# Optimization experiments

Hardware: AMD Instinct MI355X
Metric: run time of the kernel (lower is better)

## Reference

```python
import jax, jax.numpy as jnp
import numpy as np

N_NODES = 100000
N_EDGES = 1600000
IN_FEAT = 256
HIDDEN = 64
N_CLASSES = 16


def gcn_conv(x, edge_index, W, b):
    """PyG GCNConv: add self-loops, symmetric normalization, linear+aggregate."""
    n = x.shape[0]
    src, dst = edge_index[0], edge_index[1]
    loops = jnp.arange(n, dtype=src.dtype)
    src = jnp.concatenate([src, loops])
    dst = jnp.concatenate([dst, loops])
    # in-degree on graph with self-loops
    deg = jax.ops.segment_sum(jnp.ones(src.shape[0], dtype=x.dtype), dst, num_segments=n)
    dinv = jnp.where(deg > 0, jax.lax.rsqrt(deg), 0.0)
    h = x @ W                                  # [N, out]
    norm = dinv[src] * dinv[dst]               # [E+N]
    msg = h[src] * norm[:, None]                # gather + scale (memory-bound)
    out = jax.ops.segment_sum(msg, dst, num_segments=n)  # scatter-add
    return out + b


def setup_inputs() -> dict:
    key = jax.random.key(0)
    ks = jax.random.split(key, 5)
    x = jax.random.normal(ks[0], (N_NODES, IN_FEAT), dtype=jnp.float32)
    edge_index = jax.random.randint(ks[1], (2, N_EDGES), 0, N_NODES, dtype=jnp.int64)
    W1 = jax.random.normal(ks[2], (IN_FEAT, HIDDEN), dtype=jnp.float32) * (1.0 / np.sqrt(IN_FEAT))
    b1 = jnp.zeros((HIDDEN,), dtype=jnp.float32)
    W2 = jax.random.normal(ks[3], (HIDDEN, N_CLASSES), dtype=jnp.float32) * (1.0 / np.sqrt(HIDDEN))
    b2 = jnp.zeros((N_CLASSES,), dtype=jnp.float32)
    return {"x": x, "edge_index": edge_index, "W1": W1, "b1": b1, "W2": W2, "b2": b2}


def reference(x, edge_index, W1, b1, W2, b2):
    h = gcn_conv(x, edge_index, W1, b1)
    h = jax.nn.relu(h)
    # dropout p=0.5 is identity in eval mode (training=False)
    out = gcn_conv(h, edge_index, W2, b2)
    return out
```

## Files before the change

### kernel.cpp

```cpp
#include <hip/hip_runtime.h>

#define NN 100000
#define NE 1600000
#define FIN 256
#define FH 64
#define FC 16

#define NPB 512
#define NBKT ((NN + NPB - 1) / NPB)
#define NBLK 256
#define CHUNK (NE / NBLK)
#define CAP 12288
#define NB_GEMM1 ((NN + 127) / 128)

typedef int v2i __attribute__((ext_vector_type(2)));
typedef int v4i __attribute__((ext_vector_type(4)));
typedef short s16x8 __attribute__((ext_vector_type(8)));
typedef float f32x4 __attribute__((ext_vector_type(4)));
typedef _Float16 h16x8 __attribute__((ext_vector_type(8)));
typedef _Float16 h16x4 __attribute__((ext_vector_type(4)));

__device__ __forceinline__ float4 add4(float4 a, float4 v) {
    a.x += v.x; a.y += v.y; a.z += v.z; a.w += v.w;
    return a;
}
__device__ __forceinline__ float4 xor_add4(float4 r, int m) {
    r.x += __shfl_xor(r.x, m, 64); r.y += __shfl_xor(r.y, m, 64);
    r.z += __shfl_xor(r.z, m, 64); r.w += __shfl_xor(r.w, m, 64);
    return r;
}
__device__ __forceinline__ h16x8 hz8() {
    h16x8 p;
    #pragma unroll
    for (int i = 0; i < 8; i++) p[i] = (_Float16)0.0f;
    return p;
}
__device__ __forceinline__ h16x4 hz4() {
    h16x4 p;
    #pragma unroll
    for (int i = 0; i < 4; i++) p[i] = (_Float16)0.0f;
    return p;
}

__device__ __forceinline__ unsigned short bf16rne(float f) {
    unsigned u = __float_as_uint(f);
    u += 0x7FFFu + ((u >> 16) & 1u);
    return (unsigned short)(u >> 16);
}
__device__ __forceinline__ void split8(const float* f, s16x8& hi, s16x8& lo) {
    #pragma unroll
    for (int i = 0; i < 8; i++) {
        unsigned u = __float_as_uint(f[i]);
        unsigned short h = (unsigned short)((u + 0x7FFFu + ((u >> 16) & 1u)) >> 16);
        float l = f[i] - __uint_as_float((unsigned)h << 16);
        unsigned ul = __float_as_uint(l);
        hi[i] = (short)h;
        lo[i] = (short)((ul + 0x7FFFu + ((ul >> 16) & 1u)) >> 16);
    }
}
__device__ __forceinline__ int is64(const int* __restrict__ ei) {
    return (ei[1] == 0) & (ei[3] == 0) & (ei[5] == 0) & (ei[7] == 0);
}

__global__ __launch_bounds__(256) void histprep_k(const int* __restrict__ ei,
                                                  const float* __restrict__ W,
                                                  unsigned short* __restrict__ Whi,
                                                  unsigned short* __restrict__ Wlo,
                                                  int* __restrict__ cnt) {
    const int b = blockIdx.x, t = threadIdx.x;
    if (b < 8) {
        int slot = b * 256 + t;
        int l = slot & 63;
        int c = (slot >> 6) & 3;
        int s = slot >> 8;
        int k0 = s * 32 + (l >> 4) * 8;
        int col = c * 16 + (l & 15);
        #pragma unroll
        for (int i = 0; i < 8; i++) {
            float f = W[(k0 + i) * FH + col];
            unsigned short h = bf16rne(f);
            float lres = f - __uint_as_float((unsigned)h << 16);
            Whi[slot * 8 + i] = h;
            Wlo[slot * 8 + i] = bf16rne(lres);
        }
        return;
    }
    __shared__ int hist[NBKT];
    const int blk = b - 8;
    for (int j = t; j < NBKT; j += 256) hist[j] = 0;
    __syncthreads();
    int f = is64(ei);
    int base = blk * CHUNK;
    if (f) {
        for (int i = t; i < CHUNK; i += 256) {
            v2i p = *(const v2i*)&ei[2 * (NE + base + i)];
            atomicAdd(&hist[p.x >> 9], 1);
        }
    } else {
        for (int i = t; i < CHUNK; i += 256) {
            int d = ei[NE + base + i];
            atomicAdd(&hist[d >> 9], 1);
        }
    }
    __syncthreads();
    for (int j = t; j < NBKT; j += 256) cnt[j * NBLK + blk] = hist[j];
}

__global__ __launch_bounds__(1024) void scanoff_k(int* __restrict__ cnt,
                                                  int* __restrict__ bucketBase) {
    __shared__ int s[1024];
    const int t = threadIdx.x;
    const int SEG = (NBKT * NBLK) / 1024;
    int base = t * SEG;
    int sum = 0;
    for (int i = 0; i < SEG; i++) sum += cnt[base + i];
    s[t] = sum; __syncthreads();
    for (int off = 1; off < 1024; off <<= 1) {
        int u = (t >= off) ? s[t - off] : 0;
        __syncthreads();
        s[t] += u;
        __syncthreads();
    }
    int run = s[t] - sum;
    for (int i = 0; i < SEG; i++) {
        int g = base + i;
        int v = cnt[g];
        cnt[g] = run;
        if ((g & (NBLK - 1)) == 0) bucketBase[g / NBLK] = run;
        run += v;
    }
    if (t == 0) bucketBase[NBKT] = NE;
}

__global__ __launch_bounds__(256, 4) void scatgemm_k(const int* __restrict__ ei,
                                                     const int* __restrict__ cnt,
                                                     int* __restrict__ sorted,
                                                     const float* __restrict__ x,
                                                     const unsigned short* __restrict__ Whi,
                                                     const unsigned short* __restrict__ Wlo,
                                                     _Float16* __restrict__ h1h) {
    __shared__ int stash[CHUNK];
    __shared__ unsigned short bkt[CHUNK];
    __shared__ int lhist[NBKT];
    __shared__ int lstart[NBKT];
    __shared__ int lcur[NBKT];
    __shared__ int sred[256];
    const int b = blockIdx.x, t = threadIdx.x;
    if (b >= NB_GEMM1) {
        const int blk = b - NB_GEMM1;
        for (int j = t; j < NBKT; j += 256) lhist[j] = 0;
        __syncthreads();
        int f = is64(ei);
        int base = blk * CHUNK;
        if (f) {
            for (int i = t; i < CHUNK; i += 256) {
                v2i p = *(const v2i*)&ei[2 * (NE + base + i)];
                atomicAdd(&lhist[p.x >> 9], 1);
            }
        } else {
            for (int i = t; i < CHUNK; i += 256)
                atomicAdd(&lhist[ei[NE + base + i] >> 9], 1);
        }
        __syncthreads();
        int v = (t < NBKT) ? lhist[t] : 0;
        sred[t] = v; __syncthreads();
        for (int off = 1; off < 256; off <<= 1) {
            int u = (t >= off) ? sred[t - off] : 0;
            __syncthreads();
            sred[t] += u;
            __syncthreads();
        }
        if (t < NBKT) { lstart[t] = sred[t] - v; lcur[t] = sred[t] - v; }
        __syncthreads();
        if (f) {
            for (int i = t; i < CHUNK; i += 256) {
                int e = base + i;
                v2i ps = *(const v2i*)&ei[2 * e];
                v2i pd = *(const v2i*)&ei[2 * (NE + e)];
                int s = ps.x, d = pd.x;
                int bk = d >> 9;
                int pos = atomicAdd(&lcur[bk], 1);
                stash[pos] = s | ((d & (NPB - 1)) << 17);
                bkt[pos] = (unsigned short)bk;
            }
        } else {
            for (int i = t; i < CHUNK; i += 256) {
                int e = base + i;
                int s = ei[e], d = ei[NE + e];
                int bk = d >> 9;
                int pos = atomicAdd(&lcur[bk], 1);
                stash[pos] = s | ((d & (NPB - 1)) << 17);
                bkt[pos] = (unsigned short)bk;
            }
        }
        __syncthreads();
        for (int i = t; i < CHUNK; i += 256) {
            int bk = bkt[i];
            int g = cnt[bk * NBLK + blk] + (i - lstart[bk]);
            sorted[g] = stash[i];
        }
        return;
    }
    const int lane = t & 63;
    const int wid = t >> 6;
    const int mb = b * 128 + wid * 32;
    const int lr = lane & 15;
    const int lk = (lane >> 4) * 8;

    int ra0 = mb + lr;
    int ra1 = mb + 16 + lr;
    const float* pa0 = x + (size_t)(ra0 < NN ? ra0 : NN - 1) * FIN + lk;
    const float* pa1 = x + (size_t)(ra1 < NN ? ra1 : NN - 1) * FIN + lk;

    f32x4 acc[2][4] = {};

    for (int s = 0; s < 8; s++) {
        float fa0[8], fa1[8];
        float4 q;
        q = *(const float4*)(pa0 + s * 32);
        fa0[0] = q.x; fa0[1] = q.y; fa0[2] = q.z; fa0[3] = q.w;
        q = *(const float4*)(pa0 + s * 32 + 4);
        fa0[4] = q.x; fa0[5] = q.y; fa0[6] = q.z; fa0[7] = q.w;
        q = *(const float4*)(pa1 + s * 32);
        fa1[0] = q.x; fa1[1] = q.y; fa1[2] = q.z; fa1[3] = q.w;
        q = *(const float4*)(pa1 + s * 32 + 4);
        fa1[4] = q.x; fa1[5] = q.y; fa1[6] = q.z; fa1[7] = q.w;

        s16x8 a0h, a0l, a1h, a1l;
        split8(fa0, a0h, a0l);
        split8(fa1, a1h, a1l);

        #pragma unroll
        for (int c = 0; c < 4; c++) {
            s16x8 wh = *(const s16x8*)&Whi[((s * 4 + c) * 64 + lane) * 8];
            s16x8 wl = *(const s16x8*)&Wlo[((s * 4 + c) * 64 + lane) * 8];
            acc[0][c] = __builtin_amdgcn_mfma_f32_16x16x32_bf16(a0h, wh, acc[0][c], 0, 0, 0);
            acc[0][c] = __builtin_amdgcn_mfma_f32_16x16x32_bf16(a0l, wh, acc[0][c], 0, 0, 0);
            acc[0][c] = __builtin_amdgcn_mfma_f32_16x16x32_bf16(a0h, wl, acc[0][c], 0, 0, 0);
            acc[1][c] = __builtin_amdgcn_mfma_f32_16x16x32_bf16(a1h, wh, acc[1][c], 0, 0, 0);
            acc[1][c] = __builtin_amdgcn_mfma_f32_16x16x32_bf16(a1l, wh, acc[1][c], 0, 0, 0);
            acc[1][c] = __builtin_amdgcn_mfma_f32_16x16x32_bf16(a1h, wl, acc[1][c], 0, 0, 0);
        }
    }
    #pragma unroll
    for (int r = 0; r < 2; r++) {
        int rowb = mb + 16 * r + (lane >> 4) * 4;
        #pragma unroll
        for (int v = 0; v < 4; v++) {
            int row = rowb + v;
            if (row < NN) {
                #pragma unroll
                for (int c = 0; c < 4; c++)
                    h1h[(size_t)row * FH + 16 * c + lr] = (_Float16)acc[r][c][v];
            }
        }
    }
}

__global__ __launch_bounds__(256) void bucket_k(const int* __restrict__ sorted,
                                                const int* __restrict__ bucketBase,
                                                int* __restrict__ csr,
                                                int* __restrict__ row_start,
                                                float* __restrict__ dinv,
                                                _Float16* __restrict__ h1h) {
    __shared__ int stash[CAP];
    __shared__ int hist[NPB];
    __shared__ int startl[NPB];
    __shared__ int cursor[NPB];
    __shared__ int ss[256];
    const int t = threadIdx.x, b = blockIdx.x;
    const int nb0 = b * NPB;
    const int ncnt = (NN - nb0 < NPB) ? (NN - nb0) : NPB;
    const int ebase = bucketBase[b];
    const int ecnt = bucketBase[b + 1] - ebase;

    hist[t] = 0; hist[t + 256] = 0;
    __syncthreads();
    for (int i = t; i < ecnt; i += 256) {
        int v = sorted[ebase + i];
        if (i < CAP) stash[i] = v;
        atomicAdd(&hist[v >> 17], 1);
    }
    __syncthreads();
    int a = hist[2 * t], c = hist[2 * t + 1];
    int p = a + c;
    ss[t] = p; __syncthreads();
    for (int off = 1; off < 256; off <<= 1) {
        int u = (t >= off) ? ss[t - off] : 0;
        __syncthreads();
        ss[t] += u;
        __syncthreads();
    }
    int ex = ss[t] - p;
    startl[2 * t] = ex;       startl[2 * t + 1] = ex + a;
    cursor[2 * t] = ex;       cursor[2 * t + 1] = ex + a;
    __syncthreads();
    for (int j = t; j < ncnt; j += 256) {
        row_start[nb0 + j] = ebase + startl[j];
        dinv[nb0 + j] = rsqrtf((float)(hist[j] + 1));
    }
    if (b == 0 && t == 0) row_start[NN] = NE;
    for (int i = t; i < ecnt; i += 256) {
        int v = (i < CAP) ? stash[i] : sorted[ebase + i];
        int dl = v >> 17;
        int r = atomicAdd(&cursor[dl], 1);
        csr[ebase + r] = v & 0x1FFFF;
    }
    h16x8* hp = (h16x8*)h1h;
    for (int q = t; q < ncnt * 8; q += 256) {
        int rl = q >> 3;
        _Float16 dvh = (_Float16)rsqrtf((float)(hist[rl] + 1));
        h16x8 v = hp[(size_t)(nb0 + rl) * 8 + (q & 7)];
        #pragma unroll
        for (int i = 0; i < 8; i++) v[i] = v[i] * dvh;
        hp[(size_t)(nb0 + rl) * 8 + (q & 7)] = v;
    }
}

__global__ __launch_bounds__(256) void agg1g_k(const int* __restrict__ csr,
                                               const int* __restrict__ row_start,
                                               const _Float16* __restrict__ h1h,
                                               const float* __restrict__ dinv,
                                               const float* __restrict__ b1,
                                               const float* __restrict__ W2,
                                               _Float16* __restrict__ h2h) {
    __shared__ float sW2[FH * FC];
    __shared__ float sp[4][FH];
    const int t = threadIdx.x;
    #pragma unroll
    for (int i = 0; i < 4; i++) sW2[t + 256 * i] = W2[t + 256 * i];
    __syncthreads();

    const int wid = t >> 6;
    const int n = blockIdx.x * 4 + wid;
    const int lane = t & 63;
    if (n >= NN) return;
    const int sg = lane >> 3;
    const int fl = lane & 7;
    const h16x8* hp = (const h16x8*)h1h;
    int s0 = row_start[n], s1 = row_start[n + 1];
    float facc[8] = {};
    for (int j0 = s0; j0 < s1; j0 += 64) {
        int idx = j0 + lane;
        int sl = (idx < s1) ? csr[idx] : 0;
        int cnt = s1 - j0; if (cnt > 64) cnt = 64;
        h16x8 pA = hz8(), pB = hz8();
        int j = 0;
        for (; j + 16 <= cnt; j += 16) {
            int eA = __shfl(sl, j + sg, 64);
            int eB = __shfl(sl, j + 8 + sg, 64);
            pA += hp[eA * 8 + fl];
            pB += hp[eB * 8 + fl];
        }
        if (j + 8 <= cnt) {
            int eA = __shfl(sl, j + sg, 64);
            pA += hp[eA * 8 + fl];
            j += 8;
        }
        int rem = cnt - j;
        if (rem > 0) {
            int jj = j + (sg < rem ? sg : 0);
            int eA = __shfl(sl, jj, 64);
            h16x8 v = hp[eA * 8 + fl];
            if (sg < rem) pB += v;
        }
        #pragma unroll
        for (int i = 0; i < 8; i++)
            facc[i] += (float)pA[i] + (float)pB[i];
    }
    #pragma unroll
    for (int i = 0; i < 8; i++) {
        float r = facc[i];
        r += __shfl_xor(r, 8, 64);
        r += __shfl_xor(r, 16, 64);
        r += __shfl_xor(r, 32, 64);
        facc[i] = r;
    }
    float dn = dinv[n];
    if (sg == 0) {
        h16x8 sv = hp[n * 8 + fl];
        float4 p0, p1;
        float4 bq0 = *(const float4*)&b1[fl * 8];
        float4 bq1 = *(const float4*)&b1[fl * 8 + 4];
        p0.x = fmaxf(fmaf(facc[0] + (float)sv[0], dn, bq0.x), 0.f);
        p0.y = fmaxf(fmaf(facc[1] + (float)sv[1], dn, bq0.y), 0.f);
        p0.z = fmaxf(fmaf(facc[2] + (float)sv[2], dn, bq0.z), 0.f);
        p0.w = fmaxf(fmaf(facc[3] + (float)sv[3], dn, bq0.w), 0.f);
        p1.x = fmaxf(fmaf(facc[4] + (float)sv[4], dn, bq1.x), 0.f);
        p1.y = fmaxf(fmaf(facc[5] + (float)sv[5], dn, bq1.y), 0.f);
        p1.z = fmaxf(fmaf(facc[6] + (float)sv[6], dn, bq1.z), 0.f);
        p1.w = fmaxf(fmaf(facc[7] + (float)sv[7], dn, bq1.w), 0.f);
        *(float4*)&sp[wid][fl * 8] = p0;
        *(float4*)&sp[wid][fl * 8 + 4] = p1;
    }
    __builtin_amdgcn_s_waitcnt(0);
    if (lane < FC) {
        float o = 0.f;
        #pragma unroll 8
        for (int k = 0; k < FH; k++)
            o = fmaf(sp[wid][k], sW2[k * FC + lane], o);
        h2h[n * FC + lane] = (_Float16)(o * dn);
    }
}

__global__ __launch_bounds__(256) void agg2_k(const int* __restrict__ csr,
                                              const int* __restrict__ row_start,
                                              const _Float16* __restrict__ h2h,
                                              const float* __restrict__ dinv,
                                              const float* __restrict__ b2,
                                              float* __restrict__ out) {
    const int t = threadIdx.x;
    int n = blockIdx.x * 16 + (t >> 4);
    int l16 = t & 15;
    int base = t & 48;
    int q = (t >> 2) & 3;
    int c = t & 3;
    if (n >= NN) return;
    const h16x4* hp = (const h16x4*)h2h;
    int s0 = row_start[n], s1 = row_start[n + 1];
    h16x4 pA = hz4(), pB = hz4(), pC = hz4(), pD = hz4();
    for (int j0 = s0; j0 < s1; j0 += 16) {
        int idx = j0 + l16;
        int sl = (idx < s1) ? csr[idx] : 0;
        int cnt = s1 - j0; if (cnt > 16) cnt = 16;
        int j = 0;
        if (j + 16 <= cnt) {
            int eA = __shfl(sl, base + j + q, 64);
            int eB = __shfl(sl, base + j + 4 + q, 64);
            int eC = __shfl(sl, base + j + 8 + q, 64);
            int eD = __shfl(sl, base + j + 12 + q, 64);
            pA += hp[eA * 4 + c];
            pB += hp[eB * 4 + c];
            pC += hp[eC * 4 + c];
            pD += hp[eD * 4 + c];
            j += 16;
        }
        if (j + 8 <= cnt) {
            int eA = __shfl(sl, base + j + q, 64);
            int eB = __shfl(sl, base + j + 4 + q, 64);
            pA += hp[eA * 4 + c];
            pB += hp[eB * 4 + c];
            j += 8;
        }
        if (j + 4 <= cnt) {
            int eA = __shfl(sl, base + j + q, 64);
            pA += hp[eA * 4 + c];
            j += 4;
        }
        int rem = cnt - j;
        if (rem > 0) {
            int jj = base + j + (q < rem ? q : 0);
            int eA = __shfl(sl, jj, 64);
            h16x4 v = hp[eA * 4 + c];
            if (q < rem) pD += v;
        }
    }
    float4 A = make_float4((float)pA[0] + (float)pB[0] + (float)pC[0] + (float)pD[0],
                           (float)pA[1] + (float)pB[1] + (float)pC[1] + (float)pD[1],
                           (float)pA[2] + (float)pB[2] + (float)pC[2] + (float)pD[2],
                           (float)pA[3] + (float)pB[3] + (float)pC[3] + (float)pD[3]);
    float4 r = xor_add4(A, 4);
    r = xor_add4(r, 8);
    if (q == 0) {
        float dn = dinv[n];
        h16x4 sv = hp[n * 4 + c];
        float4 bq = *(const float4*)&b2[c * 4];
        float4 p;
        p.x = fmaf(r.x + (float)sv[0], dn, bq.x);
        p.y = fmaf(r.y + (float)sv[1], dn, bq.y);
        p.z = fmaf(r.z + (float)sv[2], dn, bq.z);
        p.w = fmaf(r.w + (float)sv[3], dn, bq.w);
        *(float4*)&out[n * FC + c * 4] = p;
    }
}

extern "C" void kernel_launch(void* const* d_in, const int* in_sizes, int n_in,
                              void* d_out, int out_size, void* d_ws, size_t ws_size,
                              hipStream_t stream) {
    const float* x  = (const float*)d_in[0];
    const int*   ei = (const int*)d_in[1];
    const float* W1 = (const float*)d_in[2];
    const float* b1 = (const float*)d_in[3];
    const float* W2 = (const float*)d_in[4];
    const float* b2 = (const float*)d_in[5];
    float* out = (float*)d_out;

    char* ws = (char*)d_ws;
    int*   row_start  = (int*)(ws + 0);
    float* dinv       = (float*)(ws + 512ull * 1024);
    int*   bucketBase = (int*)(ws + 960ull * 1024);
    unsigned short* Whi = (unsigned short*)(ws + 1024ull * 1024);
    unsigned short* Wlo = (unsigned short*)(ws + 1088ull * 1024);
    int*   cnt        = (int*)(ws + 1152ull * 1024);
    int*   csr        = (int*)(ws + 2048ull * 1024);
    int*   sorted     = (int*)(ws + 9216ull * 1024);
    _Float16* h1h     = (_Float16*)(ws + 16384ull * 1024);
    _Float16* h2h     = (_Float16*)(ws + 30720ull * 1024);

    histprep_k<<<8 + NBLK, 256, 0, stream>>>(ei, W1, Whi, Wlo, cnt);
    scanoff_k<<<1, 1024, 0, stream>>>(cnt, bucketBase);
    scatgemm_k<<<NB_GEMM1 + NBLK, 256, 0, stream>>>(ei, cnt, sorted, x, Whi, Wlo, h1h);
    bucket_k<<<NBKT, 256, 0, stream>>>(sorted, bucketBase, csr, row_start, dinv, h1h);
    agg1g_k<<<(NN + 3) / 4, 256, 0, stream>>>(csr, row_start, h1h, dinv, b1, W2, h2h);
    agg2_k<<<(NN + 15) / 16, 256, 0, stream>>>(csr, row_start, h2h, dinv, b2, out);
}
```

Baseline: 388.5 us.

## Parallelize bucket offset scan and simplify gather loops in aggregation kernels

Replaces the single-block 1024-thread offset scan with three kernels: a per-bucket reduce, a small scan over bucket totals, and a per-bucket row scan, so the scan work spreads across many blocks. The aggregation kernels now load CSR indices directly per lane instead of staging them through wave shuffles. The layer-1 kernel also moves the W2 projection into registers with shuffle reductions, dropping the shared-memory staging and the serial 64-step dot product. In exchange there are two extra kernel launches and redundant CSR index loads per lane.

```diff
diff --git a/kernel.cpp b/kernel.cpp
--- a/kernel.cpp
+++ b/kernel.cpp
@@ -14,21 +14,12 @@
 #define NB_GEMM1 ((NN + 127) / 128)
 
 typedef int v2i __attribute__((ext_vector_type(2)));
-typedef int v4i __attribute__((ext_vector_type(4)));
 typedef short s16x8 __attribute__((ext_vector_type(8)));
 typedef float f32x4 __attribute__((ext_vector_type(4)));
 typedef _Float16 h16x8 __attribute__((ext_vector_type(8)));
 typedef _Float16 h16x4 __attribute__((ext_vector_type(4)));
-
-__device__ __forceinline__ float4 add4(float4 a, float4 v) {
-    a.x += v.x; a.y += v.y; a.z += v.z; a.w += v.w;
-    return a;
-}
-__device__ __forceinline__ float4 xor_add4(float4 r, int m) {
-    r.x += __shfl_xor(r.x, m, 64); r.y += __shfl_xor(r.y, m, 64);
-    r.z += __shfl_xor(r.z, m, 64); r.w += __shfl_xor(r.w, m, 64);
-    return r;
-}
+typedef _Float16 h16x2 __attribute__((ext_vector_type(2)));
+
 __device__ __forceinline__ h16x8 hz8() {
     h16x8 p;
     #pragma unroll
@@ -106,30 +97,48 @@
     for (int j = t; j < NBKT; j += 256) cnt[j * NBLK + blk] = hist[j];
 }
 
-__global__ __launch_bounds__(1024) void scanoff_k(int* __restrict__ cnt,
-                                                  int* __restrict__ bucketBase) {
-    __shared__ int s[1024];
-    const int t = threadIdx.x;
-    const int SEG = (NBKT * NBLK) / 1024;
-    int base = t * SEG;
-    int sum = 0;
-    for (int i = 0; i < SEG; i++) sum += cnt[base + i];
-    s[t] = sum; __syncthreads();
-    for (int off = 1; off < 1024; off <<= 1) {
+__global__ __launch_bounds__(256) void bsum_k(const int* __restrict__ cnt,
+                                              int* __restrict__ bucketTot) {
+    __shared__ int red[256];
+    int b = blockIdx.x, t = threadIdx.x;
+    red[t] = cnt[b * NBLK + t];
+    __syncthreads();
+    for (int off = 128; off > 0; off >>= 1) {
+        if (t < off) red[t] += red[t + off];
+        __syncthreads();
+    }
+    if (t == 0) bucketTot[b] = red[0];
+}
+
+__global__ __launch_bounds__(256) void bscan_k(const int* __restrict__ bucketTot,
+                                               int* __restrict__ bucketBase) {
+    __shared__ int s[256];
+    int t = threadIdx.x;
+    int v = (t < NBKT) ? bucketTot[t] : 0;
+    s[t] = v; __syncthreads();
+    for (int off = 1; off < 256; off <<= 1) {
         int u = (t >= off) ? s[t - off] : 0;
         __syncthreads();
         s[t] += u;
         __syncthreads();
     }
-    int run = s[t] - sum;
-    for (int i = 0; i < SEG; i++) {
-        int g = base + i;
-        int v = cnt[g];
-        cnt[g] = run;
-        if ((g & (NBLK - 1)) == 0) bucketBase[g / NBLK] = run;
-        run += v;
-    }
+    if (t < NBKT) bucketBase[t] = s[t] - v;
     if (t == 0) bucketBase[NBKT] = NE;
+}
+
+__global__ __launch_bounds__(256) void brow_k(int* __restrict__ cnt,
+                                              const int* __restrict__ bucketBase) {
+    __shared__ int s[256];
+    int b = blockIdx.x, t = threadIdx.x;
+    int v = cnt[b * NBLK + t];
+    s[t] = v; __syncthreads();
+    for (int off = 1; off < 256; off <<= 1) {
+        int u = (t >= off) ? s[t - off] : 0;
+        __syncthreads();
+        s[t] += u;
+        __syncthreads();
+    }
+    cnt[b * NBLK + t] = bucketBase[b] + s[t] - v;
 }
 
 __global__ __launch_bounds__(256, 4) void scatgemm_k(const int* __restrict__ ei,
@@ -324,82 +333,58 @@
                                                const float* __restrict__ b1,
                                                const float* __restrict__ W2,
                                                _Float16* __restrict__ h2h) {
-    __shared__ float sW2[FH * FC];
-    __shared__ float sp[4][FH];
     const int t = threadIdx.x;
-    #pragma unroll
-    for (int i = 0; i < 4; i++) sW2[t + 256 * i] = W2[t + 256 * i];
-    __syncthreads();
-
     const int wid = t >> 6;
-    const int n = blockIdx.x * 4 + wid;
     const int lane = t & 63;
-    if (n >= NN) return;
     const int sg = lane >> 3;
     const int fl = lane & 7;
+    float w2r0[8], w2r1[8], br[8];
+    #pragma unroll
+    for (int i = 0; i < 8; i++) {
+        float2 w = *(const float2*)&W2[(fl * 8 + i) * FC + 2 * sg];
+        w2r0[i] = w.x; w2r1[i] = w.y;
+        br[i] = b1[fl * 8 + i];
+    }
+    const int n = blockIdx.x * 4 + wid;
+    if (n >= NN) return;
     const h16x8* hp = (const h16x8*)h1h;
     int s0 = row_start[n], s1 = row_start[n + 1];
-    float facc[8] = {};
-    for (int j0 = s0; j0 < s1; j0 += 64) {
-        int idx = j0 + lane;
-        int sl = (idx < s1) ? csr[idx] : 0;
-        int cnt = s1 - j0; if (cnt > 64) cnt = 64;
-        h16x8 pA = hz8(), pB = hz8();
-        int j = 0;
-        for (; j + 16 <= cnt; j += 16) {
-            int eA = __shfl(sl, j + sg, 64);
-            int eB = __shfl(sl, j + 8 + sg, 64);
-            pA += hp[eA * 8 + fl];
-            pB += hp[eB * 8 + fl];
-        }
-        if (j + 8 <= cnt) {
-            int eA = __shfl(sl, j + sg, 64);
-            pA += hp[eA * 8 + fl];
-            j += 8;
-        }
-        int rem = cnt - j;
-        if (rem > 0) {
-            int jj = j + (sg < rem ? sg : 0);
-            int eA = __shfl(sl, jj, 64);
-            h16x8 v = hp[eA * 8 + fl];
-            if (sg < rem) pB += v;
-        }
-        #pragma unroll
-        for (int i = 0; i < 8; i++)
-            facc[i] += (float)pA[i] + (float)pB[i];
-    }
+    h16x8 pA = hz8(), pB = hz8();
+    for (int j = s0; j < s1; j += 16) {
+        int e1 = j + sg, e2 = j + 8 + sg;
+        int c1 = csr[(e1 < s1) ? e1 : s1 - 1];
+        int c2 = csr[(e2 < s1) ? e2 : s1 - 1];
+        h16x8 vA = hp[(size_t)c1 * 8 + fl];
+        h16x8 vB = hp[(size_t)c2 * 8 + fl];
+        if (e1 < s1) pA += vA;
+        if (e2 < s1) pB += vB;
+    }
+    float facc[8];
+    #pragma unroll
+    for (int i = 0; i < 8; i++) facc[i] = (float)pA[i] + (float)pB[i];
     #pragma unroll
     for (int i = 0; i < 8; i++) {
-        float r = facc[i];
-        r += __shfl_xor(r, 8, 64);
-        r += __shfl_xor(r, 16, 64);
-        r += __shfl_xor(r, 32, 64);
-        facc[i] = r;
+        facc[i] += __shfl_xor(facc[i], 8, 64);
+        facc[i] += __shfl_xor(facc[i], 16, 64);
+        facc[i] += __shfl_xor(facc[i], 32, 64);
     }
     float dn = dinv[n];
-    if (sg == 0) {
-        h16x8 sv = hp[n * 8 + fl];
-        float4 p0, p1;
-        float4 bq0 = *(const float4*)&b1[fl * 8];
-        float4 bq1 = *(const float4*)&b1[fl * 8 + 4];
-        p0.x = fmaxf(fmaf(facc[0] + (float)sv[0], dn, bq0.x), 0.f);
-        p0.y = fmaxf(fmaf(facc[1] + (float)sv[1], dn, bq0.y), 0.f);
-        p0.z = fmaxf(fmaf(facc[2] + (float)sv[2], dn, bq0.z), 0.f);
-        p0.w = fmaxf(fmaf(facc[3] + (float)sv[3], dn, bq0.w), 0.f);
-        p1.x = fmaxf(fmaf(facc[4] + (float)sv[4], dn, bq1.x), 0.f);
-        p1.y = fmaxf(fmaf(facc[5] + (float)sv[5], dn, bq1.y), 0.f);
-        p1.z = fmaxf(fmaf(facc[6] + (float)sv[6], dn, bq1.z), 0.f);
-        p1.w = fmaxf(fmaf(facc[7] + (float)sv[7], dn, bq1.w), 0.f);
-        *(float4*)&sp[wid][fl * 8] = p0;
-        *(float4*)&sp[wid][fl * 8 + 4] = p1;
-    }
-    __builtin_amdgcn_s_waitcnt(0);
-    if (lane < FC) {
-        float o = 0.f;
-        #pragma unroll 8
-        for (int k = 0; k < FH; k++)
-            o = fmaf(sp[wid][k], sW2[k * FC + lane], o);
-        h2h[n * FC + lane] = (_Float16)(o * dn);
+    h16x8 sv = hp[(size_t)n * 8 + fl];
+    float o0 = 0.f, o1 = 0.f;
+    #pragma unroll
+    for (int i = 0; i < 8; i++) {
+        float pi = fmaxf(fmaf(facc[i] + (float)sv[i], dn, br[i]), 0.f);
+        o0 = fmaf(pi, w2r0[i], o0);
+        o1 = fmaf(pi, w2r1[i], o1);
+    }
+    o0 += __shfl_xor(o0, 1, 64); o1 += __shfl_xor(o1, 1, 64);
+    o0 += __shfl_xor(o0, 2, 64); o1 += __shfl_xor(o1, 2, 64);
+    o0 += __shfl_xor(o0, 4, 64); o1 += __shfl_xor(o1, 4, 64);
+    if (fl == 0) {
+        h16x2 r;
+        r[0] = (_Float16)(o0 * dn);
+        r[1] = (_Float16)(o1 * dn);
+        *(h16x2*)&h2h[(size_t)n * FC + 2 * sg] = r;
     }
 }
 
@@ -410,67 +395,40 @@
                                               const float* __restrict__ b2,
                                               float* __restrict__ out) {
     const int t = threadIdx.x;
-    int n = blockIdx.x * 16 + (t >> 4);
-    int l16 = t & 15;
-    int base = t & 48;
-    int q = (t >> 2) & 3;
-    int c = t & 3;
+    const int n = blockIdx.x * 16 + (t >> 4);
+    const int q = (t >> 2) & 3;
+    const int c = t & 3;
+    float4 bq = *(const float4*)&b2[c * 4];
     if (n >= NN) return;
     const h16x4* hp = (const h16x4*)h2h;
     int s0 = row_start[n], s1 = row_start[n + 1];
-    h16x4 pA = hz4(), pB = hz4(), pC = hz4(), pD = hz4();
-    for (int j0 = s0; j0 < s1; j0 += 16) {
-        int idx = j0 + l16;
-        int sl = (idx < s1) ? csr[idx] : 0;
-        int cnt = s1 - j0; if (cnt > 16) cnt = 16;
-        int j = 0;
-        if (j + 16 <= cnt) {
-            int eA = __shfl(sl, base + j + q, 64);
-            int eB = __shfl(sl, base + j + 4 + q, 64);
-            int eC = __shfl(sl, base + j + 8 + q, 64);
-            int eD = __shfl(sl, base + j + 12 + q, 64);
-            pA += hp[eA * 4 + c];
-            pB += hp[eB * 4 + c];
-            pC += hp[eC * 4 + c];
-            pD += hp[eD * 4 + c];
-            j += 16;
-        }
-        if (j + 8 <= cnt) {
-            int eA = __shfl(sl, base + j + q, 64);
-            int eB = __shfl(sl, base + j + 4 + q, 64);
-            pA += hp[eA * 4 + c];
-            pB += hp[eB * 4 + c];
-            j += 8;
-        }
-        if (j + 4 <= cnt) {
-            int eA = __shfl(sl, base + j + q, 64);
-            pA += hp[eA * 4 + c];
-            j += 4;
-        }
-        int rem = cnt - j;
-        if (rem > 0) {
-            int jj = base + j + (q < rem ? q : 0);
-            int eA = __shfl(sl, jj, 64);
-            h16x4 v = hp[eA * 4 + c];
-            if (q < rem) pD += v;
-        }
-    }
-    float4 A = make_float4((float)pA[0] + (float)pB[0] + (float)pC[0] + (float)pD[0],
-                           (float)pA[1] + (float)pB[1] + (float)pC[1] + (float)pD[1],
-                           (float)pA[2] + (float)pB[2] + (float)pC[2] + (float)pD[2],
-                           (float)pA[3] + (float)pB[3] + (float)pC[3] + (float)pD[3]);
-    float4 r = xor_add4(A, 4);
-    r = xor_add4(r, 8);
+    h16x4 pA = hz4(), pB = hz4();
+    for (int j = s0; j < s1; j += 8) {
+        int e1 = j + q, e2 = j + 4 + q;
+        int c1 = csr[(e1 < s1) ? e1 : s1 - 1];
+        int c2 = csr[(e2 < s1) ? e2 : s1 - 1];
+        h16x4 vA = hp[(size_t)c1 * 4 + c];
+        h16x4 vB = hp[(size_t)c2 * 4 + c];
+        if (e1 < s1) pA += vA;
+        if (e2 < s1) pB += vB;
+    }
+    float r0 = (float)pA[0] + (float)pB[0];
+    float r1 = (float)pA[1] + (float)pB[1];
+    float r2 = (float)pA[2] + (float)pB[2];
+    float r3 = (float)pA[3] + (float)pB[3];
+    r0 += __shfl_xor(r0, 4, 64); r1 += __shfl_xor(r1, 4, 64);
+    r2 += __shfl_xor(r2, 4, 64); r3 += __shfl_xor(r3, 4, 64);
+    r0 += __shfl_xor(r0, 8, 64); r1 += __shfl_xor(r1, 8, 64);
+    r2 += __shfl_xor(r2, 8, 64); r3 += __shfl_xor(r3, 8, 64);
     if (q == 0) {
         float dn = dinv[n];
-        h16x4 sv = hp[n * 4 + c];
-        float4 bq = *(const float4*)&b2[c * 4];
+        h16x4 sv = hp[(size_t)n * 4 + c];
         float4 p;
-        p.x = fmaf(r.x + (float)sv[0], dn, bq.x);
-        p.y = fmaf(r.y + (float)sv[1], dn, bq.y);
-        p.z = fmaf(r.z + (float)sv[2], dn, bq.z);
-        p.w = fmaf(r.w + (float)sv[3], dn, bq.w);
-        *(float4*)&out[n * FC + c * 4] = p;
+        p.x = fmaf(r0 + (float)sv[0], dn, bq.x);
+        p.y = fmaf(r1 + (float)sv[1], dn, bq.y);
+        p.z = fmaf(r2 + (float)sv[2], dn, bq.z);
+        p.w = fmaf(r3 + (float)sv[3], dn, bq.w);
+        *(float4*)&out[(size_t)n * FC + c * 4] = p;
     }
 }
 
@@ -489,6 +447,7 @@
     int*   row_start  = (int*)(ws + 0);
     float* dinv       = (float*)(ws + 512ull * 1024);
     int*   bucketBase = (int*)(ws + 960ull * 1024);
+    int*   bucketTot  = (int*)(ws + 968ull * 1024);
     unsigned short* Whi = (unsigned short*)(ws + 1024ull * 1024);
     unsigned short* Wlo = (unsigned short*)(ws + 1088ull * 1024);
     int*   cnt        = (int*)(ws + 1152ull * 1024);
@@ -498,7 +457,9 @@
     _Float16* h2h     = (_Float16*)(ws + 30720ull * 1024);
 
     histprep_k<<<8 + NBLK, 256, 0, stream>>>(ei, W1, Whi, Wlo, cnt);
-    scanoff_k<<<1, 1024, 0, stream>>>(cnt, bucketBase);
+    bsum_k<<<NBKT, 256, 0, stream>>>(cnt, bucketTot);
+    bscan_k<<<1, 256, 0, stream>>>(bucketTot, bucketBase);
+    brow_k<<<NBKT, 256, 0, stream>>>(cnt, bucketBase);
     scatgemm_k<<<NB_GEMM1 + NBLK, 256, 0, stream>>>(ei, cnt, sorted, x, Whi, Wlo, h1h);
     bucket_k<<<NBKT, 256, 0, stream>>>(sorted, bucketBase, csr, row_start, dinv, h1h);
     agg1g_k<<<(NN + 3) / 4, 256, 0, stream>>>(csr, row_start, h1h, dinv, b1, W2, h2h);
```

Measured after the change: 376.8 us. 3.0% less time.
